# Optimization experiments

Measured on AMD Instinct MI355X. Metric: run time of the kernel, lower is better.

## Reference

```python
import jax, jax.numpy as jnp
import numpy as np
import math

SCALED = True
SUBSEQUENT_MASK = True
B, SQ, SK, D, DV = 8, 2048, 2048, 1024, 1024


def _build_mask(query_lens, key_lens, sq, sk, causal):
    # (B, Sq, Sk) boolean validity mask: rows >= q_len and cols >= k_len are masked.
    qm = jnp.arange(sq)[None, :, None] < query_lens[:, None, None]
    km = jnp.arange(sk)[None, None, :] < key_lens[:, None, None]
    mask = qm & km
    if causal:
        mask = mask & (jnp.arange(sk)[None, None, :] <= jnp.arange(sq)[None, :, None])
    return mask


def _masked_softmax(scores, mask):
    # Stable masked softmax; fully-masked rows yield exactly 0 (matches the
    # original's NaN -> 0 replacement) without producing NaNs.
    neg = jnp.finfo(scores.dtype).min
    s = jnp.where(mask, scores, neg)
    m = jnp.max(s, axis=-1, keepdims=True)
    e = jnp.where(mask, jnp.exp(s - m), jnp.zeros((), scores.dtype))
    denom = jnp.sum(e, axis=-1, keepdims=True)
    return e / jnp.where(denom == 0, jnp.ones((), scores.dtype), denom)


def setup_inputs() -> dict:
    key = jax.random.key(0)
    kq, kk, kv, kql, kkl = jax.random.split(key, 5)
    return {
        "queries": jax.random.normal(kq, (B, SQ, D), dtype=jnp.float32),
        "keys": jax.random.normal(kk, (B, SK, D), dtype=jnp.float32),
        "values": jax.random.normal(kv, (B, SK, DV), dtype=jnp.float32),
        "query_lens": jax.random.randint(kql, (B,), 1, SQ + 1),
        "key_lens": jax.random.randint(kkl, (B,), 1, SK + 1),
    }


def reference(queries, keys, values, query_lens, key_lens):
    # scores: (B, Sq, Sk)
    scores = jnp.einsum("bqd,bkd->bqk", queries, keys)
    if SCALED:
        scores = scores / math.sqrt(queries.shape[2])
    mask = _build_mask(query_lens, key_lens, queries.shape[1], keys.shape[1], SUBSEQUENT_MASK)
    weights = _masked_softmax(scores, mask)
    context = jnp.einsum("bqk,bkv->bqv", weights, values)
    return (context, weights)
```

## Files before the change

kernel.cpp:

```cpp
#include <hip/hip_runtime.h>
#include <hip/hip_bf16.h>

#define B_   8
#define SQ_  2048
#define SK_  2048
#define D_   1024
#define DV_  1024

typedef __bf16 bf16;
typedef __attribute__((ext_vector_type(4))) __bf16 bf16x4;
typedef __attribute__((ext_vector_type(8))) __bf16 bf16x8;
typedef __attribute__((ext_vector_type(4))) float  f32x4;

__global__ __launch_bounds__(256)
void scores_kernel(const float* __restrict__ Q, const float* __restrict__ K,
                   const int* __restrict__ qlens, const int* __restrict__ klens,
                   float* __restrict__ Wout)
{
    const int b  = blockIdx.z;
    const int q0 = blockIdx.y * 64;
    const int k0 = blockIdx.x * 64;
    if (k0 > q0 + 63) return;
    const int qlen = qlens[b], klen = klens[b];
    if (q0 >= qlen || k0 >= klen) return;

    __shared__ __align__(16) bf16 Qs[64][72];
    __shared__ __align__(16) bf16 Ks[64][72];

    const int tid  = threadIdx.x;
    const int lane = tid & 63;
    const int w    = tid >> 6;

    const float* Qb = Q + (size_t)b * SQ_ * D_;
    const float* Kb = K + (size_t)b * SK_ * D_;

    f32x4 acc[4] = {};

    for (int d0 = 0; d0 < D_; d0 += 64) {
        #pragma unroll
        for (int i = 0; i < 4; ++i) {
            int s   = tid + i * 256;
            int row = s >> 4;
            int c4  = (s & 15) << 2;
            const float4 qv = *(const float4*)(Qb + (size_t)(q0 + row) * D_ + d0 + c4);
            const float4 kv = *(const float4*)(Kb + (size_t)(k0 + row) * D_ + d0 + c4);
            bf16x4 qb = { (bf16)qv.x, (bf16)qv.y, (bf16)qv.z, (bf16)qv.w };
            bf16x4 kb = { (bf16)kv.x, (bf16)kv.y, (bf16)kv.z, (bf16)kv.w };
            *(bf16x4*)&Qs[row][c4] = qb;
            *(bf16x4*)&Ks[row][c4] = kb;
        }
        __syncthreads();
        #pragma unroll
        for (int kk = 0; kk < 2; ++kk) {
            const int koff = kk * 32 + ((lane >> 4) << 3);
            bf16x8 a = *(const bf16x8*)&Qs[16 * w + (lane & 15)][koff];
            #pragma unroll
            for (int c = 0; c < 4; ++c) {
                bf16x8 bb = *(const bf16x8*)&Ks[16 * c + (lane & 15)][koff];
                acc[c] = __builtin_amdgcn_mfma_f32_16x16x32_bf16(a, bb, acc[c], 0, 0, 0);
            }
        }
        __syncthreads();
    }

    float* Wb = Wout + (size_t)b * SQ_ * SK_;
    const int rbase = q0 + 16 * w + ((lane >> 4) << 2);
    const int cbase = k0 + (lane & 15);
    #pragma unroll
    for (int c = 0; c < 4; ++c) {
        #pragma unroll
        for (int r = 0; r < 4; ++r) {
            Wb[(size_t)(rbase + r) * SK_ + (cbase + 16 * c)] = acc[c][r] * 0.03125f;
        }
    }
}

__global__ __launch_bounds__(256)
void softmax_kernel(const int* __restrict__ qlens, const int* __restrict__ klens,
                    float* __restrict__ W)
{
    const int bq = blockIdx.x;
    const int b  = bq >> 11;
    const int q  = bq & 2047;
    const int qlen = qlens[b], klen = klens[b];
    int kmax = 0;
    if (q < qlen) kmax = min(klen, q + 1);

    float* row = W + (size_t)bq * SK_;
    const int tid = threadIdx.x;

    float s[8];
    float m = -INFINITY;
    #pragma unroll
    for (int i = 0; i < 8; ++i) {
        int k = tid + i * 256;
        s[i] = (k < kmax) ? row[k] : -INFINITY;
        m = fmaxf(m, s[i]);
    }
    #pragma unroll
    for (int off = 32; off > 0; off >>= 1) m = fmaxf(m, __shfl_xor(m, off, 64));
    __shared__ float red[4];
    if ((tid & 63) == 0) red[tid >> 6] = m;
    __syncthreads();
    m = fmaxf(fmaxf(red[0], red[1]), fmaxf(red[2], red[3]));
    __syncthreads();

    float e[8];
    float sum = 0.f;
    #pragma unroll
    for (int i = 0; i < 8; ++i) {
        int k = tid + i * 256;
        e[i] = (k < kmax) ? __expf(s[i] - m) : 0.f;
        sum += e[i];
    }
    #pragma unroll
    for (int off = 32; off > 0; off >>= 1) sum += __shfl_xor(sum, off, 64);
    if ((tid & 63) == 0) red[tid >> 6] = sum;
    __syncthreads();
    sum = red[0] + red[1] + red[2] + red[3];

    const float inv = (sum > 0.f) ? (1.f / sum) : 0.f;
    #pragma unroll
    for (int i = 0; i < 8; ++i) row[tid + i * 256] = e[i] * inv;
}

__global__ __launch_bounds__(256)
void context_kernel(const float* __restrict__ W, const float* __restrict__ V,
                    const int* __restrict__ klens, float* __restrict__ Out)
{
    const int b  = blockIdx.z;
    const int q0 = blockIdx.y * 64;
    const int n0 = blockIdx.x * 64;
    const int klen = klens[b];
    const int kend = min(q0 + 64, (klen + 63) & ~63);

    __shared__ __align__(16) bf16 Ws[64][72];
    __shared__ __align__(16) bf16 Vs[64][72];

    const int tid  = threadIdx.x;
    const int lane = tid & 63;
    const int w    = tid >> 6;

    const float* Wb = W + (size_t)b * SQ_ * SK_;
    const float* Vb = V + (size_t)b * SK_ * DV_;

    f32x4 acc[4] = {};

    for (int k0 = 0; k0 < kend; k0 += 64) {
        #pragma unroll
        for (int i = 0; i < 4; ++i) {
            int s   = tid + i * 256;
            int row = s >> 4;
            int c4  = (s & 15) << 2;
            const float4 wv = *(const float4*)(Wb + (size_t)(q0 + row) * SK_ + k0 + c4);
            bf16x4 wb = { (bf16)wv.x, (bf16)wv.y, (bf16)wv.z, (bf16)wv.w };
            *(bf16x4*)&Ws[row][c4] = wb;
            const float4 vv = *(const float4*)(Vb + (size_t)(k0 + row) * DV_ + n0 + c4);
            Vs[c4 + 0][row] = (bf16)vv.x;
            Vs[c4 + 1][row] = (bf16)vv.y;
            Vs[c4 + 2][row] = (bf16)vv.z;
            Vs[c4 + 3][row] = (bf16)vv.w;
        }
        __syncthreads();
        #pragma unroll
        for (int kk = 0; kk < 2; ++kk) {
            const int koff = kk * 32 + ((lane >> 4) << 3);
            bf16x8 a = *(const bf16x8*)&Ws[16 * w + (lane & 15)][koff];
            #pragma unroll
            for (int c = 0; c < 4; ++c) {
                bf16x8 bb = *(const bf16x8*)&Vs[16 * c + (lane & 15)][koff];
                acc[c] = __builtin_amdgcn_mfma_f32_16x16x32_bf16(a, bb, acc[c], 0, 0, 0);
            }
        }
        __syncthreads();
    }

    float* Ob = Out + (size_t)b * SQ_ * DV_;
    const int rbase = q0 + 16 * w + ((lane >> 4) << 2);
    const int cbase = n0 + (lane & 15);
    #pragma unroll
    for (int c = 0; c < 4; ++c) {
        #pragma unroll
        for (int r = 0; r < 4; ++r) {
            Ob[(size_t)(rbase + r) * DV_ + (cbase + 16 * c)] = acc[c][r];
        }
    }
}

extern "C" void kernel_launch(void* const* d_in, const int* in_sizes, int n_in,
                              void* d_out, int out_size, void* d_ws, size_t ws_size,
                              hipStream_t stream) {
    (void)in_sizes; (void)n_in; (void)out_size; (void)d_ws; (void)ws_size;
    const float* Q     = (const float*)d_in[0];
    const float* K     = (const float*)d_in[1];
    const float* V     = (const float*)d_in[2];
    const int*   qlens = (const int*)d_in[3];
    const int*   klens = (const int*)d_in[4];

    float* ctx = (float*)d_out;
    float* wts = ctx + (size_t)B_ * SQ_ * DV_;

    dim3 g1(SK_ / 64, SQ_ / 64, B_);
    scores_kernel<<<g1, 256, 0, stream>>>(Q, K, qlens, klens, wts);

    softmax_kernel<<<dim3(B_ * SQ_), 256, 0, stream>>>(qlens, klens, wts);

    dim3 g3(DV_ / 64, SQ_ / 64, B_);
    context_kernel<<<g3, 256, 0, stream>>>(wts, V, klens, ctx);
}
```

Baseline: 584.9 us.

## Enlarge GEMM tiles to 128x128 with 4x4 MFMA per warp; vectorize softmax

Both the scores and context GEMMs now use 128x128 block tiles, with each wave computing a 64x64 subtile of 4x4 MFMA accumulators. This raises operand reuse from shared memory and cuts global reloads of Q/K/W/V. The V tile is now loaded with each thread gathering 8 consecutive k values for one column and writing one packed vector to LDS, replacing scalar transposed LDS stores. Softmax now uses float4 loads and stores. Costs are more registers per thread, larger LDS use, and coarser skipping of masked tiles.

```diff
diff --git a/kernel.cpp b/kernel.cpp
--- a/kernel.cpp
+++ b/kernel.cpp
@@ -18,27 +18,28 @@
                    float* __restrict__ Wout)
 {
     const int b  = blockIdx.z;
-    const int q0 = blockIdx.y * 64;
-    const int k0 = blockIdx.x * 64;
-    if (k0 > q0 + 63) return;
+    const int q0 = blockIdx.y * 128;
+    const int k0 = blockIdx.x * 128;
+    if (k0 > q0 + 127) return;
     const int qlen = qlens[b], klen = klens[b];
     if (q0 >= qlen || k0 >= klen) return;
 
-    __shared__ __align__(16) bf16 Qs[64][72];
-    __shared__ __align__(16) bf16 Ks[64][72];
+    __shared__ __align__(16) bf16 Qs[128][72];
+    __shared__ __align__(16) bf16 Ks[128][72];
 
     const int tid  = threadIdx.x;
     const int lane = tid & 63;
     const int w    = tid >> 6;
+    const int wq   = w >> 1, wk = w & 1;
 
     const float* Qb = Q + (size_t)b * SQ_ * D_;
     const float* Kb = K + (size_t)b * SK_ * D_;
 
-    f32x4 acc[4] = {};
+    f32x4 acc[4][4] = {};
 
     for (int d0 = 0; d0 < D_; d0 += 64) {
         #pragma unroll
-        for (int i = 0; i < 4; ++i) {
+        for (int i = 0; i < 8; ++i) {
             int s   = tid + i * 256;
             int row = s >> 4;
             int c4  = (s & 15) << 2;
@@ -53,26 +54,32 @@
         #pragma unroll
         for (int kk = 0; kk < 2; ++kk) {
             const int koff = kk * 32 + ((lane >> 4) << 3);
-            bf16x8 a = *(const bf16x8*)&Qs[16 * w + (lane & 15)][koff];
-            #pragma unroll
-            for (int c = 0; c < 4; ++c) {
-                bf16x8 bb = *(const bf16x8*)&Ks[16 * c + (lane & 15)][koff];
-                acc[c] = __builtin_amdgcn_mfma_f32_16x16x32_bf16(a, bb, acc[c], 0, 0, 0);
-            }
+            bf16x8 a[4], bb[4];
+            #pragma unroll
+            for (int m = 0; m < 4; ++m)
+                a[m] = *(const bf16x8*)&Qs[64 * wq + 16 * m + (lane & 15)][koff];
+            #pragma unroll
+            for (int n = 0; n < 4; ++n)
+                bb[n] = *(const bf16x8*)&Ks[64 * wk + 16 * n + (lane & 15)][koff];
+            #pragma unroll
+            for (int m = 0; m < 4; ++m)
+                #pragma unroll
+                for (int n = 0; n < 4; ++n)
+                    acc[m][n] = __builtin_amdgcn_mfma_f32_16x16x32_bf16(a[m], bb[n], acc[m][n], 0, 0, 0);
         }
         __syncthreads();
     }
 
     float* Wb = Wout + (size_t)b * SQ_ * SK_;
-    const int rbase = q0 + 16 * w + ((lane >> 4) << 2);
-    const int cbase = k0 + (lane & 15);
-    #pragma unroll
-    for (int c = 0; c < 4; ++c) {
-        #pragma unroll
-        for (int r = 0; r < 4; ++r) {
-            Wb[(size_t)(rbase + r) * SK_ + (cbase + 16 * c)] = acc[c][r] * 0.03125f;
-        }
-    }
+    const int rb = q0 + 64 * wq + ((lane >> 4) << 2);
+    const int cb = k0 + 64 * wk + (lane & 15);
+    #pragma unroll
+    for (int m = 0; m < 4; ++m)
+        #pragma unroll
+        for (int n = 0; n < 4; ++n)
+            #pragma unroll
+            for (int r = 0; r < 4; ++r)
+                Wb[(size_t)(rb + 16 * m + r) * SK_ + (cb + 16 * n)] = acc[m][n][r] * 0.03125f;
 }
 
 __global__ __launch_bounds__(256)
@@ -86,16 +93,22 @@
     int kmax = 0;
     if (q < qlen) kmax = min(klen, q + 1);
 
-    float* row = W + (size_t)bq * SK_;
+    float4* row = (float4*)(W + (size_t)bq * SK_);
     const int tid = threadIdx.x;
 
-    float s[8];
+    float4 x[2];
     float m = -INFINITY;
     #pragma unroll
-    for (int i = 0; i < 8; ++i) {
-        int k = tid + i * 256;
-        s[i] = (k < kmax) ? row[k] : -INFINITY;
-        m = fmaxf(m, s[i]);
+    for (int i = 0; i < 2; ++i) {
+        int v4 = tid + i * 256;
+        x[i] = row[v4];
+        int kb = v4 << 2;
+        float* xe = (float*)&x[i];
+        #pragma unroll
+        for (int e = 0; e < 4; ++e) {
+            if (kb + e >= kmax) xe[e] = -INFINITY;
+            m = fmaxf(m, xe[e]);
+        }
     }
     #pragma unroll
     for (int off = 32; off > 0; off >>= 1) m = fmaxf(m, __shfl_xor(m, off, 64));
@@ -105,13 +118,16 @@
     m = fmaxf(fmaxf(red[0], red[1]), fmaxf(red[2], red[3]));
     __syncthreads();
 
-    float e[8];
     float sum = 0.f;
     #pragma unroll
-    for (int i = 0; i < 8; ++i) {
-        int k = tid + i * 256;
-        e[i] = (k < kmax) ? __expf(s[i] - m) : 0.f;
-        sum += e[i];
+    for (int i = 0; i < 2; ++i) {
+        float* xe = (float*)&x[i];
+        #pragma unroll
+        for (int e = 0; e < 4; ++e) {
+            float ev = (xe[e] == -INFINITY) ? 0.f : __expf(xe[e] - m);
+            xe[e] = ev;
+            sum += ev;
+        }
     }
     #pragma unroll
     for (int off = 32; off > 0; off >>= 1) sum += __shfl_xor(sum, off, 64);
@@ -121,7 +137,11 @@
 
     const float inv = (sum > 0.f) ? (1.f / sum) : 0.f;
     #pragma unroll
-    for (int i = 0; i < 8; ++i) row[tid + i * 256] = e[i] * inv;
+    for (int i = 0; i < 2; ++i) {
+        float* xe = (float*)&x[i];
+        float4 o = { xe[0] * inv, xe[1] * inv, xe[2] * inv, xe[3] * inv };
+        row[tid + i * 256] = o;
+    }
 }
 
 __global__ __launch_bounds__(256)
@@ -129,62 +149,77 @@
                     const int* __restrict__ klens, float* __restrict__ Out)
 {
     const int b  = blockIdx.z;
-    const int q0 = blockIdx.y * 64;
-    const int n0 = blockIdx.x * 64;
+    const int q0 = blockIdx.y * 128;
+    const int n0 = blockIdx.x * 128;
     const int klen = klens[b];
-    const int kend = min(q0 + 64, (klen + 63) & ~63);
-
-    __shared__ __align__(16) bf16 Ws[64][72];
-    __shared__ __align__(16) bf16 Vs[64][72];
+    const int kend = min(q0 + 128, (klen + 63) & ~63);
+
+    __shared__ __align__(16) bf16 Ws[128][72];
+    __shared__ __align__(16) bf16 Vs[128][72];
 
     const int tid  = threadIdx.x;
     const int lane = tid & 63;
     const int w    = tid >> 6;
+    const int wq   = w >> 1, wn = w & 1;
 
     const float* Wb = W + (size_t)b * SQ_ * SK_;
     const float* Vb = V + (size_t)b * SK_ * DV_;
 
-    f32x4 acc[4] = {};
-
-    for (int k0 = 0; k0 < kend; k0 += 64) {
-        #pragma unroll
-        for (int i = 0; i < 4; ++i) {
+    f32x4 acc[4][4] = {};
+
+    for (int kk0 = 0; kk0 < kend; kk0 += 64) {
+        #pragma unroll
+        for (int i = 0; i < 8; ++i) {
             int s   = tid + i * 256;
             int row = s >> 4;
             int c4  = (s & 15) << 2;
-            const float4 wv = *(const float4*)(Wb + (size_t)(q0 + row) * SK_ + k0 + c4);
+            const float4 wv = *(const float4*)(Wb + (size_t)(q0 + row) * SK_ + kk0 + c4);
             bf16x4 wb = { (bf16)wv.x, (bf16)wv.y, (bf16)wv.z, (bf16)wv.w };
             *(bf16x4*)&Ws[row][c4] = wb;
-            const float4 vv = *(const float4*)(Vb + (size_t)(k0 + row) * DV_ + n0 + c4);
-            Vs[c4 + 0][row] = (bf16)vv.x;
-            Vs[c4 + 1][row] = (bf16)vv.y;
-            Vs[c4 + 2][row] = (bf16)vv.z;
-            Vs[c4 + 3][row] = (bf16)vv.w;
+        }
+        #pragma unroll
+        for (int i = 0; i < 4; ++i) {
+            int t   = tid + i * 256;
+            int n   = t & 127;
+            int oct = t >> 7;
+            float v[8];
+            #pragma unroll
+            for (int j = 0; j < 8; ++j)
+                v[j] = Vb[(size_t)(kk0 + oct * 8 + j) * DV_ + n0 + n];
+            bf16x8 vb = { (bf16)v[0], (bf16)v[1], (bf16)v[2], (bf16)v[3],
+                          (bf16)v[4], (bf16)v[5], (bf16)v[6], (bf16)v[7] };
+            *(bf16x8*)&Vs[n][oct * 8] = vb;
         }
         __syncthreads();
         #pragma unroll
         for (int kk = 0; kk < 2; ++kk) {
             const int koff = kk * 32 + ((lane >> 4) << 3);
-            bf16x8 a = *(const bf16x8*)&Ws[16 * w + (lane & 15)][koff];
-            #pragma unroll
-            for (int c = 0; c < 4; ++c) {
-                bf16x8 bb = *(const bf16x8*)&Vs[16 * c + (lane & 15)][koff];
-                acc[c] = __builtin_amdgcn_mfma_f32_16x16x32_bf16(a, bb, acc[c], 0, 0, 0);
-            }
+            bf16x8 a[4], bb[4];
+            #pragma unroll
+            for (int m = 0; m < 4; ++m)
+                a[m] = *(const bf16x8*)&Ws[64 * wq + 16 * m + (lane & 15)][koff];
+            #pragma unroll
+            for (int n = 0; n < 4; ++n)
+                bb[n] = *(const bf16x8*)&Vs[64 * wn + 16 * n + (lane & 15)][koff];
+            #pragma unroll
+            for (int m = 0; m < 4; ++m)
+                #pragma unroll
+                for (int n = 0; n < 4; ++n)
+                    acc[m][n] = __builtin_amdgcn_mfma_f32_16x16x32_bf16(a[m], bb[n], acc[m][n], 0, 0, 0);
         }
         __syncthreads();
     }
 
     float* Ob = Out + (size_t)b * SQ_ * DV_;
-    const int rbase = q0 + 16 * w + ((lane >> 4) << 2);
-    const int cbase = n0 + (lane & 15);
-    #pragma unroll
-    for (int c = 0; c < 4; ++c) {
-        #pragma unroll
-        for (int r = 0; r < 4; ++r) {
-            Ob[(size_t)(rbase + r) * DV_ + (cbase + 16 * c)] = acc[c][r];
-        }
-    }
+    const int rb = q0 + 64 * wq + ((lane >> 4) << 2);
+    const int cb = n0 + 64 * wn + (lane & 15);
+    #pragma unroll
+    for (int m = 0; m < 4; ++m)
+        #pragma unroll
+        for (int n = 0; n < 4; ++n)
+            #pragma unroll
+            for (int r = 0; r < 4; ++r)
+                Ob[(size_t)(rb + 16 * m + r) * DV_ + (cb + 16 * n)] = acc[m][n][r];
 }
 
 extern "C" void kernel_launch(void* const* d_in, const int* in_sizes, int n_in,
@@ -200,11 +235,11 @@
     float* ctx = (float*)d_out;
     float* wts = ctx + (size_t)B_ * SQ_ * DV_;
 
-    dim3 g1(SK_ / 64, SQ_ / 64, B_);
+    dim3 g1(SK_ / 128, SQ_ / 128, B_);
     scores_kernel<<<g1, 256, 0, stream>>>(Q, K, qlens, klens, wts);
 
     softmax_kernel<<<dim3(B_ * SQ_), 256, 0, stream>>>(qlens, klens, wts);
 
-    dim3 g3(DV_ / 64, SQ_ / 64, B_);
+    dim3 g3(DV_ / 128, SQ_ / 128, B_);
     context_kernel<<<g3, 256, 0, stream>>>(wts, V, klens, ctx);
 }
```

Result: faster. 509.5 us (-12.9%).
